# Performance work log

Measured on AMD Instinct MI355X. Metric: run time of the kernel, lower is better.

Reference implementation:

```python
import jax, jax.numpy as jnp
import numpy as np

N, IN_DIM, OUT_DIM, BATCH = 8192, 128, 128, 4


def _glorot(key, shape):
    lim = float(np.sqrt(6.0 / (shape[0] + shape[1])))
    return jax.random.uniform(key, shape, jnp.float32, -lim, lim)


def setup_inputs() -> dict:
    key = jax.random.key(0)
    ks = jax.random.split(key, 16)
    inp = {
        "x": jax.random.normal(ks[0], (BATCH, N, IN_DIM), jnp.float32),
        "L0": jax.random.normal(ks[1], (N, N), jnp.float32) / np.sqrt(N),
        "L1": jax.random.normal(ks[2], (N, N), jnp.float32) / np.sqrt(N),
        "L2": jax.random.normal(ks[3], (N, N), jnp.float32) / np.sqrt(N),
        "L3": jax.random.normal(ks[4], (N, N), jnp.float32) / np.sqrt(N),
    }
    # 8 GCN layers: (branch b, layer l) -> W_bl, bias_bl
    kidx = 5
    for b in range(4):
        for l in range(2):
            d_in = IN_DIM if l == 0 else OUT_DIM
            inp[f"W{b}{l}"] = _glorot(ks[kidx], (d_in, OUT_DIM))
            inp[f"b{b}{l}"] = jnp.zeros((OUT_DIM,), jnp.float32)
            kidx += 1
    return inp


def _gcn_block(L, x, W, b):
    # support = L @ x  (graph propagation), then dense transform + ReLU
    support = jnp.einsum("nm,bmf->bnf", L, x)  # [B, N, F_in]
    return jax.nn.relu(support @ W + b)        # [B, N, F_out]


def reference(x, L0, L1, L2, L3,
              W00, b00, W01, b01,
              W10, b10, W11, b11,
              W20, b20, W21, b21,
              W30, b30, W31, b31):
    x0 = _gcn_block(L0, _gcn_block(L0, x, W00, b00), W01, b01)
    x1 = _gcn_block(L1, _gcn_block(L1, x, W10, b10), W11, b11)
    x2 = _gcn_block(L2, _gcn_block(L2, x, W20, b20), W21, b21)
    x3 = _gcn_block(L3, _gcn_block(L3, x, W30, b30), W31, b31)
    return (x0, x1, x2, x3)
```

## Files before the change

kernel.cpp:

```cpp
#include <hip/hip_runtime.h>
#include <stdint.h>


typedef short bf16x8 __attribute__((ext_vector_type(8)));
typedef float f32x4  __attribute__((ext_vector_type(4)));
typedef unsigned int u32x4 __attribute__((ext_vector_type(4)));
typedef float f32x16 __attribute__((ext_vector_type(16)));

static __device__ __forceinline__ unsigned short f2bf(float f) {
  __bf16 h = (__bf16)f;
  return __builtin_bit_cast(unsigned short, h);
}
static __device__ __forceinline__ unsigned int pack2(float a, float b) {
  return (unsigned int)f2bf(a) | ((unsigned int)f2bf(b) << 16);
}
static __device__ __forceinline__ bf16x8 cvt8(float4 lo, float4 hi) {
  bf16x8 r;
  r[0] = (short)f2bf(lo.x); r[1] = (short)f2bf(lo.y);
  r[2] = (short)f2bf(lo.z); r[3] = (short)f2bf(lo.w);
  r[4] = (short)f2bf(hi.x); r[5] = (short)f2bf(hi.y);
  r[6] = (short)f2bf(hi.z); r[7] = (short)f2bf(hi.w);
  return r;
}

#define GLOAD16(g, l)                                                                  \
  __builtin_amdgcn_global_load_lds((const __attribute__((address_space(1))) void*)(g), \
                                   (__attribute__((address_space(3))) void*)(l), 16, 0, 0)

struct WPtrs { const float* w[8]; };
__global__ __launch_bounds__(256)
void prep_w(WPtrs p, unsigned short* __restrict__ wt) {
  const int s = blockIdx.x;
  const float* W = p.w[s];
  unsigned short* dst = wt + s * 16384;
  for (int i = threadIdx.x; i < 16384; i += 256) {
    const int fi = i >> 7, fo = i & 127;
    dst[fo * 128 + fi] = f2bf(W[i]);
  }
}

struct LPtrs { const float* l[4]; };
__global__ __launch_bounds__(256)
void conv_l(LPtrs p, char* __restrict__ lbf) {
  __shared__ char T[32768];
  const int t = threadIdx.x, lane = t & 63, wave = t >> 6;
  const int rg = blockIdx.x, kg = blockIdx.y, br = blockIdx.z;
  const float* L = p.l[br];
  const int r0 = rg * 64, k0 = kg * 256;
  const int mt = rg >> 2, rowoff = (rg & 3) * 64, kt0 = kg * 8;
#pragma unroll
  for (int i = 0; i < 16; ++i) {
    const int rr = wave * 16 + i;
    const f32x4* src = (const f32x4*)(L + (size_t)(r0 + rr) * 8192 + k0);
    f32x4 v = __builtin_nontemporal_load(src + lane);
    const int ktl = lane >> 3;
    const int ch  = ((lane >> 1) & 3) ^ ((rr >> 1) & 3);
    uint2 pv; pv.x = pack2(v[0], v[1]); pv.y = pack2(v[2], v[3]);
    *(uint2*)(T + ktl * 4096 + rr * 64 + ch * 16 + (lane & 1) * 8) = pv;
  }
  __syncthreads();
  char* dstb = lbf + ((size_t)(br * 32 + mt) * 256 + kt0) * 16384 + rowoff * 64;
#pragma unroll
  for (int ktl = 0; ktl < 8; ++ktl) {
    u32x4 v = ((const u32x4*)(T + ktl * 4096))[t];
    __builtin_nontemporal_store(v, (u32x4*)(dstb + (size_t)ktl * 16384) + t);
  }
}

template <int AFP32>
__global__ __launch_bounds__(256)
void small_gemm(const float* __restrict__ x, const unsigned short* __restrict__ H1m,
                const unsigned short* __restrict__ WT, unsigned short* __restrict__ Z) {
  __shared__ unsigned short Sa[128 * 136];

  const int t = threadIdx.x, lane = t & 63, wave = t >> 6;
  const int l15 = lane & 15, lk = (lane >> 4) * 8;
  const int wm = (wave >> 1) * 64, wn = (wave & 1) * 64;
  const int mt = blockIdx.x, br = blockIdx.y;
  const int batch = mt >> 6, node0 = (mt & 63) * 128;

  {
    const int row = t >> 1, seg = (t & 1) * 64;
    if (AFP32) {
      const float4* src = (const float4*)(x + ((size_t)batch * 8192 + node0 + row) * 128 + seg);
      uint4* dst = (uint4*)&Sa[row * 136 + seg];
#pragma unroll
      for (int i = 0; i < 8; ++i) {
        float4 a = src[i * 2], b = src[i * 2 + 1];
        uint4 v;
        v.x = pack2(a.x, a.y); v.y = pack2(a.z, a.w);
        v.z = pack2(b.x, b.y); v.w = pack2(b.z, b.w);
        dst[i] = v;
      }
    } else {
      const uint4* src = (const uint4*)(H1m + ((size_t)(br * 4 + batch) * 8192 + node0 + row) * 128 + seg);
      uint4* dst = (uint4*)&Sa[row * 136 + seg];
#pragma unroll
      for (int i = 0; i < 8; ++i) dst[i] = src[i];
    }
  }
  __syncthreads();

  const unsigned short* WTb = WT + (size_t)(2 * br + (AFP32 ? 0 : 1)) * 16384;
  f32x4 acc[4][4];
#pragma unroll
  for (int i = 0; i < 4; ++i)
#pragma unroll
    for (int j = 0; j < 4; ++j) acc[i][j] = f32x4{0.f, 0.f, 0.f, 0.f};

#pragma unroll
  for (int kk = 0; kk < 4; ++kk) {
    bf16x8 av[4], wv[4];
#pragma unroll
    for (int mi = 0; mi < 4; ++mi)
      av[mi] = *(const bf16x8*)&Sa[(wm + mi * 16 + l15) * 136 + kk * 32 + lk];
#pragma unroll
    for (int ni = 0; ni < 4; ++ni)
      wv[ni] = *(const bf16x8*)&WTb[(wn + ni * 16 + l15) * 128 + kk * 32 + lk];
#pragma unroll
    for (int mi = 0; mi < 4; ++mi)
#pragma unroll
      for (int ni = 0; ni < 4; ++ni)
        acc[mi][ni] = __builtin_amdgcn_mfma_f32_16x16x32_bf16(av[mi], wv[ni], acc[mi][ni], 0, 0, 0);
  }

#pragma unroll
  for (int mi = 0; mi < 4; ++mi) {
#pragma unroll
    for (int ni = 0; ni < 4; ++ni) {
      const int row0 = wm + mi * 16 + (lane >> 4) * 4;
      const int col  = wn + ni * 16 + l15;
      uint2 pv;
      pv.x = pack2(acc[mi][ni][0], acc[mi][ni][1]);
      pv.y = pack2(acc[mi][ni][2], acc[mi][ni][3]);
      *(uint2*)(Z + ((size_t)br * 512 + batch * 128 + col) * 8192 + node0 + row0) = pv;
    }
  }
}

struct BigArgs {
  const float* L[4];
  const float* bias[4];
  const unsigned short* Z;
  void* Dst;
};

#define MFMASET(AV0, AV1, AV2, AV3, BV0, BV1) do {                           \
    __builtin_amdgcn_s_setprio(1);                                           \
    c00 = __builtin_amdgcn_mfma_f32_32x32x16_bf16(AV0, BV0, c00, 0, 0, 0);   \
    c01 = __builtin_amdgcn_mfma_f32_32x32x16_bf16(AV0, BV1, c01, 0, 0, 0);   \
    c10 = __builtin_amdgcn_mfma_f32_32x32x16_bf16(AV1, BV0, c10, 0, 0, 0);   \
    c11 = __builtin_amdgcn_mfma_f32_32x32x16_bf16(AV1, BV1, c11, 0, 0, 0);   \
    c20 = __builtin_amdgcn_mfma_f32_32x32x16_bf16(AV2, BV0, c20, 0, 0, 0);   \
    c21 = __builtin_amdgcn_mfma_f32_32x32x16_bf16(AV2, BV1, c21, 0, 0, 0);   \
    c30 = __builtin_amdgcn_mfma_f32_32x32x16_bf16(AV3, BV0, c30, 0, 0, 0);   \
    c31 = __builtin_amdgcn_mfma_f32_32x32x16_bf16(AV3, BV1, c31, 0, 0, 0);   \
    __builtin_amdgcn_s_setprio(0); } while (0)

#define RDSET(ab_, bb_, s_, AV0, AV1, AV2, AV3, BV0, BV1) do {         \
    const int _ch = ((2 * (s_) + hk) ^ key4) * 16;                     \
    AV0 = *(const bf16x8*)((ab_) + aBase + _ch);                       \
    AV1 = *(const bf16x8*)((ab_) + aBase + 2048 + _ch);                \
    AV2 = *(const bf16x8*)((ab_) + aBase + 4096 + _ch);                \
    AV3 = *(const bf16x8*)((ab_) + aBase + 6144 + _ch);                \
    BV0 = *(const bf16x8*)((bb_) + bBase + _ch);                       \
    BV1 = *(const bf16x8*)((bb_) + bBase + 2048 + _ch); } while (0)

#define BIG_EPILOGUE()                                                                     \
  __syncthreads();                                                                          \
  if (LAYER == 0) {                                                                         \
    unsigned short* S16 = (unsigned short*)smem;                                            \
    _Pragma("unroll")                                                                       \
    for (int h = 0; h < 2; ++h) {                                                           \
      if (((wave >> 1) & 1) == h) {                                                         \
        EPI16(0, 0, c00); EPI16(0, 1, c01);                                                 \
        EPI16(1, 0, c10); EPI16(1, 1, c11);                                                 \
        EPI16(2, 0, c20); EPI16(2, 1, c21);                                                 \
        EPI16(3, 0, c30); EPI16(3, 1, c31);                                                 \
      }                                                                                     \
      __syncthreads();                                                                      \
      const int batch = nb * 2 + h;                                                         \
      const int row = t >> 1, seg = (t & 1) * 64;                                           \
      unsigned short* Dst = (unsigned short*)a.Dst;                                         \
      const uint4* src = (const uint4*)&S16[row * 136 + seg];                               \
      uint4* dst = (uint4*)(Dst + ((size_t)(br * 4 + batch) * 8192 + mbase + row) * 128 + seg); \
      _Pragma("unroll") for (int i = 0; i < 8; ++i) dst[i] = src[i];                        \
      __syncthreads();                                                                      \
    }                                                                                       \
  } else {                                                                                  \
    float* S32 = (float*)smem;                                                              \
    _Pragma("unroll")                                                                       \
    for (int h = 0; h < 2; ++h) {                                                           \
      _Pragma("unroll")                                                                     \
      for (int rh = 0; rh < 2; ++rh) {                                                      \
        if (((wave >> 1) & 1) == h && (wave >> 2) == rh) {                                  \
          EPI32(0, 0, c00); EPI32(0, 1, c01);                                               \
          EPI32(1, 0, c10); EPI32(1, 1, c11);                                               \
          EPI32(2, 0, c20); EPI32(2, 1, c21);                                               \
          EPI32(3, 0, c30); EPI32(3, 1, c31);                                               \
        }                                                                                   \
        __syncthreads();                                                                    \
        const int batch = nb * 2 + h;                                                       \
        const int row = t >> 2, seg = (t & 3) * 32;                                         \
        float* Dst = (float*)a.Dst;                                                         \
        const float4* src = (const float4*)&S32[row * 128 + seg];                           \
        float4* dst = (float4*)(Dst + ((size_t)(br * 4 + batch) * 8192 + mbase + rh * 128 + row) * 128 + seg); \
        _Pragma("unroll") for (int i = 0; i < 8; ++i) dst[i] = src[i];                      \
        __syncthreads();                                                                    \
      }                                                                                     \
    }                                                                                       \
  }

#define EPI16(AM, BN, ACC) do {                                             \
    const int col = (wave & 1) * 64 + (BN) * 32 + l31;                      \
    const float bvv = bias[col];                                            \
    _Pragma("unroll") for (int r = 0; r < 16; ++r) {                        \
      const int row = wm + (AM) * 32 + (r & 3) + 8 * (r >> 2) + 4 * hk;     \
      S16[row * 136 + col] = f2bf(fmaxf(ACC[r] + bvv, 0.f));                \
    } } while (0)
#define EPI32(AM, BN, ACC) do {                                             \
    const int col = (wave & 1) * 64 + (BN) * 32 + l31;                      \
    const float bvv = bias[col];                                            \
    _Pragma("unroll") for (int r = 0; r < 16; ++r) {                        \
      const int lrow = (AM) * 32 + (r & 3) + 8 * (r >> 2) + 4 * hk;         \
      S32[lrow * 128 + col] = fmaxf(ACC[r] + bvv, 0.f);                     \
    } } while (0)

template <int LAYER>
__global__ __launch_bounds__(512)
void big_gemm_pc(BigArgs a, const char* __restrict__ Lbf) {
  extern __shared__ char smem[];

  const int t = threadIdx.x, lane = t & 63, wave = t >> 6;
  const int l31 = lane & 31, hk = lane >> 5;
  const int wm = (wave >> 2) * 128, wn = (wave & 3) * 64;

  const int bid = blockIdx.x;
  const int work = (bid & 7) * 32 + (bid >> 3);
  const int nb = work & 1, mt = (work >> 1) & 31, br = work >> 6;
  const int mbase = mt * 256;

  const float* bias = a.bias[br];
  const unsigned short* Zb = a.Z + (size_t)br * (512 * 8192);

  const char* aTiles = Lbf + ((size_t)(br * 32 + mt) * 256) * 16384;
  const unsigned short* bG = Zb + (size_t)(nb * 256 + wave * 32 + (lane >> 2)) * 8192
                                + ((lane & 3) ^ ((lane >> 3) & 3)) * 8;

  const int aBase = (wm + l31) * 64;
  const int bBase = (wn + l31) * 64;
  const int key4 = (l31 >> 1) & 3;

  f32x16 c00{}, c01{}, c10{}, c11{}, c20{}, c21{}, c30{}, c31{};
  bf16x8 pa0, pa1, pa2, pa3, pb0, pb1;
  bf16x8 qa0, qa1, qa2, qa3, qb0, qb1;

#define STG(T_) do {                                                          \
    const char* _as = aTiles + (size_t)(T_) * 16384 + wave * 2048 + lane * 16;\
    char* _ad = smem + ((T_) & 3) * 16384 + wave * 2048;                      \
    GLOAD16(_as, _ad);                                                        \
    GLOAD16(_as + 1024, _ad + 1024);                                          \
    const unsigned short* _bp = bG + (size_t)(T_) * 32;                       \
    char* _bl = smem + 65536 + ((T_) & 3) * 16384 + wave * 2048;              \
    GLOAD16(_bp, _bl);                                                        \
    GLOAD16(_bp + 16 * 8192, _bl + 1024); } while (0)

#define ITER(T_, VMSTR, DO_STG) do {                                          \
    asm volatile("s_waitcnt " VMSTR ::: "memory");                            \
    __builtin_amdgcn_s_barrier();                                             \
    if (DO_STG) STG((T_) + 3);                                                \
    const char* _ab = smem + ((T_) & 3) * 16384;                              \
    const char* _bb = smem + 65536 + ((T_) & 3) * 16384;                      \
    RDSET(_ab, _bb, 0, pa0, pa1, pa2, pa3, pb0, pb1);                         \
    RDSET(_ab, _bb, 1, qa0, qa1, qa2, qa3, qb0, qb1);                         \
    MFMASET(pa0, pa1, pa2, pa3, pb0, pb1);                                    \
    MFMASET(qa0, qa1, qa2, qa3, qb0, qb1);                                    \
  } while (0)

  STG(0); STG(1); STG(2);

  for (int T = 0; T < 252; T += 4) {
    ITER(T,     "vmcnt(8)", 1);
    ITER(T + 1, "vmcnt(8)", 1);
    ITER(T + 2, "vmcnt(8)", 1);
    ITER(T + 3, "vmcnt(8)", 1);
  }
  ITER(252, "vmcnt(8)", 1);
  ITER(253, "vmcnt(8)", 0);
  ITER(254, "vmcnt(4)", 0);
  ITER(255, "vmcnt(0)", 0);
#undef ITER
#undef STG

  BIG_EPILOGUE()
}

template <int LAYER>
__global__ __launch_bounds__(512, 2)
void big_gemm_rs(BigArgs a) {
  extern __shared__ char smem[];

  const int t = threadIdx.x, lane = t & 63, wave = t >> 6;
  const int l31 = lane & 31, hk = lane >> 5;
  const int wm = (wave >> 2) * 128, wn = (wave & 3) * 64;

  const int bid = blockIdx.x;
  const int work = (bid & 7) * 32 + (bid >> 3);
  const int nb = work & 1, mt = (work >> 1) & 31, br = work >> 6;
  const int mbase = mt * 256;

  const float* A = a.L[br];
  const float* bias = a.bias[br];
  const unsigned short* Zb = a.Z + (size_t)br * (512 * 8192);

  const int arow = t >> 1, ah = t & 1;
  const float* aG = A + (size_t)(mbase + arow) * 8192 + ah * 16;
  const int c0 = 2 * ah, akey = (arow >> 1) & 3;
  char* aRowL = smem + arow * 64;
  const unsigned short* bG = Zb + (size_t)(nb * 256 + wave * 32 + (lane >> 2)) * 8192
                                + ((lane & 3) ^ ((lane >> 3) & 3)) * 8;
  char* bWave = smem + 32768 + wave * 2048;

  const int aBase = (wm + l31) * 64;
  const int bBase = (wn + l31) * 64;
  const int key4 = (l31 >> 1) & 3;

  f32x16 c00{}, c01{}, c10{}, c11{}, c20{}, c21{}, c30{}, c31{};
  float4 s0[4], s1[4], s2[4];
  bf16x8 pa0, pa1, pa2, pa3, pb0, pb1;
  bf16x8 qa0, qa1, qa2, qa3, qb0, qb1;

#define GLB(T_) do {                                                   \
    const unsigned short* _bp = bG + (size_t)(T_) * 32;                \
    char* _bl = bWave + ((T_) & 3) * 16384;                            \
    GLOAD16(_bp, _bl);                                                 \
    GLOAD16(_bp + 16 * 8192, _bl + 1024); } while (0)
#define LOADA(T_, R) do {                                              \
    const float* _ap = aG + (size_t)(T_) * 32;                         \
    R[0] = *(const float4*)(_ap);                                      \
    R[1] = *(const float4*)(_ap + 4);                                  \
    R[2] = *(const float4*)(_ap + 8);                                  \
    R[3] = *(const float4*)(_ap + 12); } while (0)
#define WRITEA(T_, R) do {                                             \
    char* _al = aRowL + (((T_) & 1)) * 16384;                          \
    *(bf16x8*)(_al + ((c0 ^ akey) * 16))       = cvt8(R[0], R[1]);     \
    *(bf16x8*)(_al + (((c0 + 1) ^ akey) * 16)) = cvt8(R[2], R[3]); } while (0)
#define ITER(T_, SLOAD, SWRITE, VMSTR, DO_STAGE, DO_WRITE) do {        \
    asm volatile("s_waitcnt " VMSTR ::: "memory");                     \
    asm volatile("s_waitcnt lgkmcnt(0)" ::: "memory");                 \
    __builtin_amdgcn_s_barrier();                                      \
    if (DO_STAGE) { GLB((T_) + 3); LOADA((T_) + 3, SLOAD); }           \
    const char* _ab = smem + ((T_) & 1) * 16384;                       \
    const char* _bb = smem + 32768 + ((T_) & 3) * 16384;               \
    RDSET(_ab, _bb, 0, pa0, pa1, pa2, pa3, pb0, pb1);                  \
    MFMASET(pa0, pa1, pa2, pa3, pb0, pb1);                             \
    if (DO_WRITE) WRITEA((T_) + 1, SWRITE);                            \
    RDSET(_ab, _bb, 1, qa0, qa1, qa2, qa3, qb0, qb1);                  \
    MFMASET(qa0, qa1, qa2, qa3, qb0, qb1);                             \
  } while (0)

  GLB(0); LOADA(0, s0);
  GLB(1); LOADA(1, s1);
  GLB(2); LOADA(2, s2);
  WRITEA(0, s0);

  for (int T = 0; T < 252; T += 3) {
    ITER(T,     s0, s1, "vmcnt(12)", 1, 1);
    ITER(T + 1, s1, s2, "vmcnt(12)", 1, 1);
    ITER(T + 2, s2, s0, "vmcnt(12)", 1, 1);
  }
  ITER(252, s0, s1, "vmcnt(12)", 1, 1);
  ITER(253, s0, s2, "vmcnt(12)", 0, 1);
  ITER(254, s0, s0, "vmcnt(6)",  0, 1);
  ITER(255, s0, s0, "vmcnt(0)",  0, 0);
#undef ITER
#undef WRITEA
#undef LOADA
#undef GLB

  BIG_EPILOGUE()
}

extern "C" void kernel_launch(void* const* d_in, const int* in_sizes, int n_in,
                              void* d_out, int out_size, void* d_ws, size_t ws_size,
                              hipStream_t stream) {
  const float* x = (const float*)d_in[0];
  unsigned short* Z   = (unsigned short*)d_ws;
  unsigned short* H1m = Z + (size_t)4 * 512 * 8192;
  unsigned short* WT  = H1m + (size_t)4 * 4 * 8192 * 128;
  char* Lbf = (char*)(WT + 8 * 16384);
  float* out = (float*)d_out;

  const size_t NEED_PC = (size_t)33554432 + 33554432 + 262144 + 536870912;
  const bool use_pc = ws_size >= NEED_PC;

  static int attr_done = 0;
  if (!attr_done) {
    (void)hipFuncSetAttribute((const void*)big_gemm_pc<0>, hipFuncAttributeMaxDynamicSharedMemorySize, 131072);
    (void)hipFuncSetAttribute((const void*)big_gemm_pc<1>, hipFuncAttributeMaxDynamicSharedMemorySize, 131072);
    (void)hipFuncSetAttribute((const void*)big_gemm_rs<0>, hipFuncAttributeMaxDynamicSharedMemorySize, 98304);
    (void)hipFuncSetAttribute((const void*)big_gemm_rs<1>, hipFuncAttributeMaxDynamicSharedMemorySize, 98304);
    attr_done = 1;
  }

  WPtrs wp;
  for (int b = 0; b < 4; ++b) {
    wp.w[b * 2 + 0] = (const float*)d_in[5 + b * 4 + 0];
    wp.w[b * 2 + 1] = (const float*)d_in[5 + b * 4 + 2];
  }
  prep_w<<<8, 256, 0, stream>>>(wp, WT);

  BigArgs a0, a1;
  for (int b = 0; b < 4; ++b) {
    a0.L[b] = (const float*)d_in[1 + b];
    a1.L[b] = (const float*)d_in[1 + b];
    a0.bias[b] = (const float*)d_in[6 + b * 4];
    a1.bias[b] = (const float*)d_in[8 + b * 4];
  }
  a0.Z = Z; a0.Dst = (void*)H1m;
  a1.Z = Z; a1.Dst = (void*)out;

  if (use_pc) {
    LPtrs lp;
    for (int b = 0; b < 4; ++b) lp.l[b] = (const float*)d_in[1 + b];
    conv_l<<<dim3(128, 32, 4), 256, 0, stream>>>(lp, Lbf);
    small_gemm<1><<<dim3(256, 4), 256, 0, stream>>>(x, nullptr, WT, Z);
    big_gemm_pc<0><<<256, 512, 131072, stream>>>(a0, Lbf);
    small_gemm<0><<<dim3(256, 4), 256, 0, stream>>>(nullptr, H1m, WT, Z);
    big_gemm_pc<1><<<256, 512, 131072, stream>>>(a1, Lbf);
  } else {
    small_gemm<1><<<dim3(256, 4), 256, 0, stream>>>(x, nullptr, WT, Z);
    big_gemm_rs<0><<<256, 512, 98304, stream>>>(a0);
    small_gemm<0><<<dim3(256, 4), 256, 0, stream>>>(nullptr, H1m, WT, Z);
    big_gemm_rs<1><<<256, 512, 98304, stream>>>(a1);
  }
}
```

Measured before the change: 924.6 us.

## Fuse second-layer weight GEMM into big GEMM epilogue and split pipeline phases

In the precomputed-bf16 path, the layer-0 big GEMM epilogue now applies ReLU, stages the activations in shared memory, and multiplies them by the layer-1 weights with MFMA. It writes the transposed Z operand for the second propagation directly, so the separate small_gemm launch and the round trip of the intermediate H1 through memory go away. The main loop is also rewritten to issue A and B tile loads in two half-phases, with barriers between LDS reads and MFMAs. The extra barriers per iteration could cost throughput, and the epilogue does more work and needs more registers.

```diff
diff --git a/kernel.cpp b/kernel.cpp
--- a/kernel.cpp
+++ b/kernel.cpp
@@ -142,6 +142,7 @@
   const float* L[4];
   const float* bias[4];
   const unsigned short* Z;
+  const unsigned short* WTall;
   void* Dst;
 };
 
@@ -165,51 +166,6 @@
     AV3 = *(const bf16x8*)((ab_) + aBase + 6144 + _ch);                \
     BV0 = *(const bf16x8*)((bb_) + bBase + _ch);                       \
     BV1 = *(const bf16x8*)((bb_) + bBase + 2048 + _ch); } while (0)
-
-#define BIG_EPILOGUE()                                                                     \
-  __syncthreads();                                                                          \
-  if (LAYER == 0) {                                                                         \
-    unsigned short* S16 = (unsigned short*)smem;                                            \
-    _Pragma("unroll")                                                                       \
-    for (int h = 0; h < 2; ++h) {                                                           \
-      if (((wave >> 1) & 1) == h) {                                                         \
-        EPI16(0, 0, c00); EPI16(0, 1, c01);                                                 \
-        EPI16(1, 0, c10); EPI16(1, 1, c11);                                                 \
-        EPI16(2, 0, c20); EPI16(2, 1, c21);                                                 \
-        EPI16(3, 0, c30); EPI16(3, 1, c31);                                                 \
-      }                                                                                     \
-      __syncthreads();                                                                      \
-      const int batch = nb * 2 + h;                                                         \
-      const int row = t >> 1, seg = (t & 1) * 64;                                           \
-      unsigned short* Dst = (unsigned short*)a.Dst;                                         \
-      const uint4* src = (const uint4*)&S16[row * 136 + seg];                               \
-      uint4* dst = (uint4*)(Dst + ((size_t)(br * 4 + batch) * 8192 + mbase + row) * 128 + seg); \
-      _Pragma("unroll") for (int i = 0; i < 8; ++i) dst[i] = src[i];                        \
-      __syncthreads();                                                                      \
-    }                                                                                       \
-  } else {                                                                                  \
-    float* S32 = (float*)smem;                                                              \
-    _Pragma("unroll")                                                                       \
-    for (int h = 0; h < 2; ++h) {                                                           \
-      _Pragma("unroll")                                                                     \
-      for (int rh = 0; rh < 2; ++rh) {                                                      \
-        if (((wave >> 1) & 1) == h && (wave >> 2) == rh) {                                  \
-          EPI32(0, 0, c00); EPI32(0, 1, c01);                                               \
-          EPI32(1, 0, c10); EPI32(1, 1, c11);                                               \
-          EPI32(2, 0, c20); EPI32(2, 1, c21);                                               \
-          EPI32(3, 0, c30); EPI32(3, 1, c31);                                               \
-        }                                                                                   \
-        __syncthreads();                                                                    \
-        const int batch = nb * 2 + h;                                                       \
-        const int row = t >> 2, seg = (t & 3) * 32;                                         \
-        float* Dst = (float*)a.Dst;                                                         \
-        const float4* src = (const float4*)&S32[row * 128 + seg];                           \
-        float4* dst = (float4*)(Dst + ((size_t)(br * 4 + batch) * 8192 + mbase + rh * 128 + row) * 128 + seg); \
-        _Pragma("unroll") for (int i = 0; i < 8; ++i) dst[i] = src[i];                      \
-        __syncthreads();                                                                    \
-      }                                                                                     \
-    }                                                                                       \
-  }
 
 #define EPI16(AM, BN, ACC) do {                                             \
     const int col = (wave & 1) * 64 + (BN) * 32 + l31;                      \
@@ -253,46 +209,129 @@
 
   f32x16 c00{}, c01{}, c10{}, c11{}, c20{}, c21{}, c30{}, c31{};
   bf16x8 pa0, pa1, pa2, pa3, pb0, pb1;
-  bf16x8 qa0, qa1, qa2, qa3, qb0, qb1;
-
-#define STG(T_) do {                                                          \
-    const char* _as = aTiles + (size_t)(T_) * 16384 + wave * 2048 + lane * 16;\
-    char* _ad = smem + ((T_) & 3) * 16384 + wave * 2048;                      \
-    GLOAD16(_as, _ad);                                                        \
-    GLOAD16(_as + 1024, _ad + 1024);                                          \
-    const unsigned short* _bp = bG + (size_t)(T_) * 32;                       \
-    char* _bl = smem + 65536 + ((T_) & 3) * 16384 + wave * 2048;              \
-    GLOAD16(_bp, _bl);                                                        \
+
+#define STGA(T_) do {                                                          \
+    const char* _as = aTiles + (size_t)(T_) * 16384 + wave * 2048 + lane * 16; \
+    char* _ad = smem + ((T_) & 3) * 16384 + wave * 2048;                       \
+    GLOAD16(_as, _ad);                                                         \
+    GLOAD16(_as + 1024, _ad + 1024); } while (0)
+#define STGB(T_) do {                                                          \
+    const unsigned short* _bp = bG + (size_t)(T_) * 32;                        \
+    char* _bl = smem + 65536 + ((T_) & 3) * 16384 + wave * 2048;               \
+    GLOAD16(_bp, _bl);                                                         \
     GLOAD16(_bp + 16 * 8192, _bl + 1024); } while (0)
 
-#define ITER(T_, VMSTR, DO_STG) do {                                          \
-    asm volatile("s_waitcnt " VMSTR ::: "memory");                            \
-    __builtin_amdgcn_s_barrier();                                             \
-    if (DO_STG) STG((T_) + 3);                                                \
-    const char* _ab = smem + ((T_) & 3) * 16384;                              \
-    const char* _bb = smem + 65536 + ((T_) & 3) * 16384;                      \
-    RDSET(_ab, _bb, 0, pa0, pa1, pa2, pa3, pb0, pb1);                         \
-    RDSET(_ab, _bb, 1, qa0, qa1, qa2, qa3, qb0, qb1);                         \
-    MFMASET(pa0, pa1, pa2, pa3, pb0, pb1);                                    \
-    MFMASET(qa0, qa1, qa2, qa3, qb0, qb1);                                    \
+#define PH(T_, S_, STG_, VM_) do {                                             \
+    const char* _ab = smem + ((T_) & 3) * 16384;                               \
+    const char* _bb = smem + 65536 + ((T_) & 3) * 16384;                       \
+    RDSET(_ab, _bb, S_, pa0, pa1, pa2, pa3, pb0, pb1);                         \
+    STG_;                                                                      \
+    VM_;                                                                       \
+    __builtin_amdgcn_s_barrier();                                              \
+    asm volatile("s_waitcnt lgkmcnt(0)" ::: "memory");                         \
+    MFMASET(pa0, pa1, pa2, pa3, pb0, pb1);                                     \
+    __builtin_amdgcn_s_barrier();                                              \
   } while (0)
 
-  STG(0); STG(1); STG(2);
-
-  for (int T = 0; T < 252; T += 4) {
-    ITER(T,     "vmcnt(8)", 1);
-    ITER(T + 1, "vmcnt(8)", 1);
-    ITER(T + 2, "vmcnt(8)", 1);
-    ITER(T + 3, "vmcnt(8)", 1);
-  }
-  ITER(252, "vmcnt(8)", 1);
-  ITER(253, "vmcnt(8)", 0);
-  ITER(254, "vmcnt(4)", 0);
-  ITER(255, "vmcnt(0)", 0);
-#undef ITER
-#undef STG
-
-  BIG_EPILOGUE()
+#define VM8  asm volatile("s_waitcnt vmcnt(8)" ::: "memory")
+#define VM4  asm volatile("s_waitcnt vmcnt(4)" ::: "memory")
+#define VM0  asm volatile("s_waitcnt vmcnt(0)" ::: "memory")
+
+  STGA(0); STGB(0); STGA(1); STGB(1); STGA(2); STGB(2);
+  VM8;
+  __builtin_amdgcn_s_barrier();
+
+  for (int T = 0; T < 252; ++T) {
+    PH(T, 0, STGA(T + 3), (void)0);
+    PH(T, 1, STGB(T + 3), VM8);
+  }
+  PH(252, 0, STGA(255), (void)0);
+  PH(252, 1, STGB(255), VM8);
+  PH(253, 0, (void)0, (void)0);
+  PH(253, 1, (void)0, VM4);
+  PH(254, 0, (void)0, (void)0);
+  PH(254, 1, (void)0, VM0);
+  PH(255, 0, (void)0, (void)0);
+  PH(255, 1, (void)0, (void)0);
+#undef PH
+#undef STGA
+#undef STGB
+
+  __syncthreads();
+
+  if (LAYER == 0) {
+    unsigned short* S16 = (unsigned short*)smem;
+    const unsigned short* W1 = a.WTall + (size_t)(2 * br + 1) * 16384;
+    unsigned short* Zo = (unsigned short*)a.Dst;
+    const int wm2 = (wave >> 2) * 128;
+    const int wn2 = (wave & 3) * 32;
+#pragma unroll
+    for (int h = 0; h < 2; ++h) {
+      if (((wave >> 1) & 1) == h) {
+        EPI16(0, 0, c00); EPI16(0, 1, c01);
+        EPI16(1, 0, c10); EPI16(1, 1, c11);
+        EPI16(2, 0, c20); EPI16(2, 1, c21);
+        EPI16(3, 0, c30); EPI16(3, 1, c31);
+      }
+      __syncthreads();
+      f32x16 z0{}, z1{}, z2{}, z3{};
+#pragma unroll
+      for (int ks = 0; ks < 8; ++ks) {
+        const int ko = ks * 32 + hk * 16;
+        const char* sb = (const char*)S16;
+        bf16x8 sa0 = *(const bf16x8*)(sb + (wm2 + l31) * 272 + ko);
+        bf16x8 sa1 = *(const bf16x8*)(sb + (wm2 + 32 + l31) * 272 + ko);
+        bf16x8 sa2 = *(const bf16x8*)(sb + (wm2 + 64 + l31) * 272 + ko);
+        bf16x8 sa3 = *(const bf16x8*)(sb + (wm2 + 96 + l31) * 272 + ko);
+        bf16x8 wv  = *(const bf16x8*)((const char*)W1 + (wn2 + l31) * 256 + ko);
+        z0 = __builtin_amdgcn_mfma_f32_32x32x16_bf16(sa0, wv, z0, 0, 0, 0);
+        z1 = __builtin_amdgcn_mfma_f32_32x32x16_bf16(sa1, wv, z1, 0, 0, 0);
+        z2 = __builtin_amdgcn_mfma_f32_32x32x16_bf16(sa2, wv, z2, 0, 0, 0);
+        z3 = __builtin_amdgcn_mfma_f32_32x32x16_bf16(sa3, wv, z3, 0, 0, 0);
+      }
+      const int batch = nb * 2 + h;
+      const int fo = wn2 + l31;
+      unsigned short* colp = Zo + ((size_t)(br * 512 + batch * 128) + fo) * 8192
+                                + mbase + wm2;
+#pragma unroll
+      for (int g = 0; g < 4; ++g) {
+        const int rb = 8 * g + 4 * hk;
+        uint2 p0, p1, p2, p3;
+        p0.x = pack2(z0[4 * g], z0[4 * g + 1]); p0.y = pack2(z0[4 * g + 2], z0[4 * g + 3]);
+        p1.x = pack2(z1[4 * g], z1[4 * g + 1]); p1.y = pack2(z1[4 * g + 2], z1[4 * g + 3]);
+        p2.x = pack2(z2[4 * g], z2[4 * g + 1]); p2.y = pack2(z2[4 * g + 2], z2[4 * g + 3]);
+        p3.x = pack2(z3[4 * g], z3[4 * g + 1]); p3.y = pack2(z3[4 * g + 2], z3[4 * g + 3]);
+        *(uint2*)(colp + rb)      = p0;
+        *(uint2*)(colp + 32 + rb) = p1;
+        *(uint2*)(colp + 64 + rb) = p2;
+        *(uint2*)(colp + 96 + rb) = p3;
+      }
+      __syncthreads();
+    }
+  } else {
+    float* S32 = (float*)smem;
+#pragma unroll
+    for (int h = 0; h < 2; ++h) {
+#pragma unroll
+      for (int rh = 0; rh < 2; ++rh) {
+        if (((wave >> 1) & 1) == h && (wave >> 2) == rh) {
+          EPI32(0, 0, c00); EPI32(0, 1, c01);
+          EPI32(1, 0, c10); EPI32(1, 1, c11);
+          EPI32(2, 0, c20); EPI32(2, 1, c21);
+          EPI32(3, 0, c30); EPI32(3, 1, c31);
+        }
+        __syncthreads();
+        const int batch = nb * 2 + h;
+        const int row = t >> 2, seg = (t & 3) * 32;
+        float* Dst = (float*)a.Dst;
+        const float4* src = (const float4*)&S32[row * 128 + seg];
+        float4* dst = (float4*)(Dst + ((size_t)(br * 4 + batch) * 8192 + mbase + rh * 128 + row) * 128 + seg);
+#pragma unroll
+        for (int i = 0; i < 8; ++i) dst[i] = src[i];
+        __syncthreads();
+      }
+    }
+  }
 }
 
 template <int LAYER>
@@ -378,7 +417,51 @@
 #undef LOADA
 #undef GLB
 
-  BIG_EPILOGUE()
+  __syncthreads();
+  if (LAYER == 0) {
+    unsigned short* S16 = (unsigned short*)smem;
+#pragma unroll
+    for (int h = 0; h < 2; ++h) {
+      if (((wave >> 1) & 1) == h) {
+        EPI16(0, 0, c00); EPI16(0, 1, c01);
+        EPI16(1, 0, c10); EPI16(1, 1, c11);
+        EPI16(2, 0, c20); EPI16(2, 1, c21);
+        EPI16(3, 0, c30); EPI16(3, 1, c31);
+      }
+      __syncthreads();
+      const int batch = nb * 2 + h;
+      const int row = t >> 1, seg = (t & 1) * 64;
+      unsigned short* Dst = (unsigned short*)a.Dst;
+      const uint4* src = (const uint4*)&S16[row * 136 + seg];
+      uint4* dst = (uint4*)(Dst + ((size_t)(br * 4 + batch) * 8192 + mbase + row) * 128 + seg);
+#pragma unroll
+      for (int i = 0; i < 8; ++i) dst[i] = src[i];
+      __syncthreads();
+    }
+  } else {
+    float* S32 = (float*)smem;
+#pragma unroll
+    for (int h = 0; h < 2; ++h) {
+#pragma unroll
+      for (int rh = 0; rh < 2; ++rh) {
+        if (((wave >> 1) & 1) == h && (wave >> 2) == rh) {
+          EPI32(0, 0, c00); EPI32(0, 1, c01);
+          EPI32(1, 0, c10); EPI32(1, 1, c11);
+          EPI32(2, 0, c20); EPI32(2, 1, c21);
+          EPI32(3, 0, c30); EPI32(3, 1, c31);
+        }
+        __syncthreads();
+        const int batch = nb * 2 + h;
+        const int row = t >> 2, seg = (t & 3) * 32;
+        float* Dst = (float*)a.Dst;
+        const float4* src = (const float4*)&S32[row * 128 + seg];
+        float4* dst = (float4*)(Dst + ((size_t)(br * 4 + batch) * 8192 + mbase + rh * 128 + row) * 128 + seg);
+#pragma unroll
+        for (int i = 0; i < 8; ++i) dst[i] = src[i];
+        __syncthreads();
+      }
+    }
+  }
 }
 
 extern "C" void kernel_launch(void* const* d_in, const int* in_sizes, int n_in,
@@ -386,8 +469,8 @@
                               hipStream_t stream) {
   const float* x = (const float*)d_in[0];
   unsigned short* Z   = (unsigned short*)d_ws;
-  unsigned short* H1m = Z + (size_t)4 * 512 * 8192;
-  unsigned short* WT  = H1m + (size_t)4 * 4 * 8192 * 128;
+  unsigned short* Z2  = Z + (size_t)4 * 512 * 8192;
+  unsigned short* WT  = Z2 + (size_t)4 * 512 * 8192;
   char* Lbf = (char*)(WT + 8 * 16384);
   float* out = (float*)d_out;
 
@@ -417,18 +500,21 @@
     a0.bias[b] = (const float*)d_in[6 + b * 4];
     a1.bias[b] = (const float*)d_in[8 + b * 4];
   }
-  a0.Z = Z; a0.Dst = (void*)H1m;
-  a1.Z = Z; a1.Dst = (void*)out;
+  a0.WTall = WT; a1.WTall = WT;
 
   if (use_pc) {
     LPtrs lp;
     for (int b = 0; b < 4; ++b) lp.l[b] = (const float*)d_in[1 + b];
     conv_l<<<dim3(128, 32, 4), 256, 0, stream>>>(lp, Lbf);
     small_gemm<1><<<dim3(256, 4), 256, 0, stream>>>(x, nullptr, WT, Z);
+    a0.Z = Z;  a0.Dst = (void*)Z2;
+    a1.Z = Z2; a1.Dst = (void*)out;
     big_gemm_pc<0><<<256, 512, 131072, stream>>>(a0, Lbf);
-    small_gemm<0><<<dim3(256, 4), 256, 0, stream>>>(nullptr, H1m, WT, Z);
     big_gemm_pc<1><<<256, 512, 131072, stream>>>(a1, Lbf);
   } else {
+    unsigned short* H1m = Z2;
+    a0.Z = Z; a0.Dst = (void*)H1m;
+    a1.Z = Z; a1.Dst = (void*)out;
     small_gemm<1><<<dim3(256, 4), 256, 0, stream>>>(x, nullptr, WT, Z);
     big_gemm_rs<0><<<256, 512, 98304, stream>>>(a0);
     small_gemm<0><<<dim3(256, 4), 256, 0, stream>>>(nullptr, H1m, WT, Z);
```

Measured after the change: 911.6 us. No clear change (-1.4%).
